# Kernel optimization log

Measured on AMD Instinct MI355X. Metric: run time of the kernel, lower is better.

The kernel has to match this reference:

```python
import jax, jax.numpy as jnp
import numpy as np

N_HEAD = 16
N_FEAT = 1024
D_K = N_FEAT // N_HEAD


def setup_inputs() -> dict:
    key = jax.random.key(0)
    ks = jax.random.split(key, 12)
    B, T, F = 4, 2048, N_FEAT
    s = 1.0 / np.sqrt(F)
    return {
        "query": jax.random.normal(ks[0], (B, T, F), dtype=jnp.float32),
        "key": jax.random.normal(ks[1], (B, T, F), dtype=jnp.float32),
        "value": jax.random.normal(ks[2], (B, T, F), dtype=jnp.float32),
        "mask": jnp.ones((B, 1, T), dtype=jnp.int32),
        "Wq": jax.random.normal(ks[3], (F, F), dtype=jnp.float32) * s,
        "bq": jax.random.normal(ks[4], (F,), dtype=jnp.float32) * 0.01,
        "Wk": jax.random.normal(ks[5], (F, F), dtype=jnp.float32) * s,
        "bk": jax.random.normal(ks[6], (F,), dtype=jnp.float32) * 0.01,
        "Wv": jax.random.normal(ks[7], (F, F), dtype=jnp.float32) * s,
        "bv": jax.random.normal(ks[8], (F,), dtype=jnp.float32) * 0.01,
        "Wo": jax.random.normal(ks[9], (F, F), dtype=jnp.float32) * s,
        "bo": jax.random.normal(ks[10], (F,), dtype=jnp.float32) * 0.01,
    }


def reference(query, key, value, mask, Wq, bq, Wk, bk, Wv, bv, Wo, bo):
    B, Tq, F = query.shape
    Tk = key.shape[1]
    h, dk = N_HEAD, D_K
    # torch nn.Linear: y = x @ W.T + b ; then view [B,T,h,dk] and transpose to [B,h,T,dk]
    q = (query @ Wq.T + bq).reshape(B, Tq, h, dk).transpose(0, 2, 1, 3)
    k = (key @ Wk.T + bk).reshape(B, Tk, h, dk).transpose(0, 2, 1, 3)
    v = (value @ Wv.T + bv).reshape(B, Tk, h, dk).transpose(0, 2, 1, 3)
    scale = 1.0 / np.sqrt(dk).astype(np.float32)
    scores = jnp.einsum("bhqd,bhkd->bhqk", q, k) * scale  # [B,h,Tq,Tk]
    # mask [B,1,Tk] -> unsqueeze(1) -> [B,1,1,Tk], True where mask == 0 (padded)
    pad = (mask[:, None, :, :] == 0)
    min_value = jnp.finfo(scores.dtype).min
    scores = jnp.where(pad, min_value, scores)
    atten = jax.nn.softmax(scores, axis=-1)
    atten = jnp.where(pad, 0.0, atten)
    # dropout_rate = 0.0 (eval): identity
    x = jnp.einsum("bhqk,bhkd->bhqd", atten, v)  # [B,h,Tq,dk]
    x = x.transpose(0, 2, 1, 3).reshape(B, Tq, h * dk)
    return x @ Wo.T + bo
```

## Files before the change

kernel.cpp:

```cpp
#include <hip/hip_runtime.h>
#include <hip/hip_bf16.h>


typedef unsigned short u16;
typedef unsigned long long u64;
typedef __attribute__((ext_vector_type(8))) short short8;
typedef __attribute__((ext_vector_type(4))) float f32x4;
typedef __attribute__((ext_vector_type(16))) float f32x16;
typedef __attribute__((ext_vector_type(4))) unsigned int u32x4;

#define GLOAD16(g, l) __builtin_amdgcn_global_load_lds( \
    (const __attribute__((address_space(1))) unsigned int*)(g), \
    (__attribute__((address_space(3))) unsigned int*)(l), 16, 0, 0)

__device__ __forceinline__ u16 f2bf(float x) {
  unsigned int u = __float_as_uint(x);
  return (u16)((u + 0x7fffu + ((u >> 16) & 1u)) >> 16);
}

__device__ __forceinline__ float fexp2(float x) {
#if __has_builtin(__builtin_amdgcn_exp2f)
  return __builtin_amdgcn_exp2f(x);
#else
  return exp2f(x);
#endif
}

__device__ __forceinline__ unsigned cvtpk(float lo, float hi) {
  unsigned r;
  asm("v_cvt_pk_bf16_f32 %0, %1, %2" : "=v"(r) : "v"(lo), "v"(hi));
  return r;
}

struct CvtArgs {
  const float* src[4];
  u16* dst[4];
};

__global__ __launch_bounds__(256) void cvt_multi(CvtArgs a, int shift) {
  const int id = blockIdx.x * 256 + threadIdx.x;
  const int seg = id >> shift;
  const int off = id & ((1 << shift) - 1);
  float4 v = ((const float4*)a.src[seg])[off];
  ushort4 o;
  o.x = f2bf(v.x); o.y = f2bf(v.y); o.z = f2bf(v.z); o.w = f2bf(v.w);
  ((ushort4*)a.dst[seg])[off] = o;
}

template <int EPI>
__global__ __launch_bounds__(256) void gemm_bt(const u16* __restrict__ A,
                                               const u16* __restrict__ Bw,
                                               const float* __restrict__ bias,
                                               void* __restrict__ Cout,
                                               float scale) {
  __shared__ u16 As[128 * 64];
  __shared__ u16 Bs[128 * 64];
  const int t = threadIdx.x;
  const int lane = t & 63;
  const int w = t >> 6;
  const int wm = w >> 1, wn = w & 1;
  const int l15 = lane & 15, l4 = lane >> 4;

  const int bid = blockIdx.x;
  const int swz = (bid & 7) * 64 + (bid >> 3);
  const int brow = swz >> 3;
  const int bcol = swz & 7;

  f32x4 acc[4][4] = {};

  const int srow = t >> 3;
  const int sbyte = (t & 7) * 16;

  for (int kt = 0; kt < 16; ++kt) {
    const int k0 = kt * 64;
    __syncthreads();
#pragma unroll
    for (int i = 0; i < 4; ++i) {
      const int r = i * 32 + srow;
      const int sb = sbyte ^ ((r & 7) << 4);
      GLOAD16((const char*)(A + (size_t)(brow * 128 + r) * 1024 + k0) + sb,
              &As[(i * 4096 + t * 16) >> 1]);
      GLOAD16((const char*)(Bw + (size_t)(bcol * 128 + r) * 1024 + k0) + sb,
              &Bs[(i * 4096 + t * 16) >> 1]);
    }
    __syncthreads();
#pragma unroll
    for (int kf = 0; kf < 2; ++kf) {
      short8 af[4], bfv[4];
#pragma unroll
      for (int mi = 0; mi < 4; ++mi) {
        const int r = wm * 64 + mi * 16 + l15;
        const int byt = r * 128 + ((kf * 64 + l4 * 16) ^ ((r & 7) << 4));
        af[mi] = *(const short8*)&As[byt >> 1];
      }
#pragma unroll
      for (int ni = 0; ni < 4; ++ni) {
        const int r = wn * 64 + ni * 16 + l15;
        const int byt = r * 128 + ((kf * 64 + l4 * 16) ^ ((r & 7) << 4));
        bfv[ni] = *(const short8*)&Bs[byt >> 1];
      }
#pragma unroll
      for (int mi = 0; mi < 4; ++mi)
#pragma unroll
        for (int ni = 0; ni < 4; ++ni)
          acc[mi][ni] = __builtin_amdgcn_mfma_f32_16x16x32_bf16(
              af[mi], bfv[ni], acc[mi][ni], 0, 0, 0);
    }
  }

#pragma unroll
  for (int ni = 0; ni < 4; ++ni) {
    const int n = bcol * 128 + wn * 64 + ni * 16 + l15;
    const float bn = bias[n];
#pragma unroll
    for (int mi = 0; mi < 4; ++mi) {
      const int mb = brow * 128 + wm * 64 + mi * 16 + l4 * 4;
#pragma unroll
      for (int r = 0; r < 4; ++r) {
        const float v = acc[mi][ni][r] + bn;
        const int m = mb + r;
        const int b_ = m >> 11, tok = m & 2047, h_ = n >> 6, d = n & 63;
        if (EPI == 0) {
          ((u16*)Cout)[(((size_t)(b_ * 16 + h_) * 2048 + tok) << 6) + d] = f2bf(v * scale);
        } else if (EPI == 2) {
          ((u16*)Cout)[(((size_t)(b_ * 16 + h_) * 64 + d) << 11) + tok] = f2bf(v);
        } else {
          ((float*)Cout)[(size_t)m * 1024 + n] = v;
        }
      }
    }
  }
}

__global__ __launch_bounds__(256, 4) void attn_fwd4(const u16* __restrict__ Q,
                                                    const u16* __restrict__ Kp,
                                                    const u16* __restrict__ Vt,
                                                    const int* __restrict__ mask,
                                                    u16* __restrict__ ctx) {
  __shared__ u16 Ks[2][64 * 64];
  __shared__ u16 Vs[2][64 * 64];

  const int t = threadIdx.x, lane = t & 63, w = t >> 6;
  const int q31 = lane & 31, hi = lane >> 5;

  const int bid = blockIdx.x;
  const int swz = (bid & 7) * 128 + (bid >> 3);
  const int bh = swz >> 4;
  const int b_ = bh >> 4, h_ = bh & 15;
  const int q0 = (swz & 15) * 128 + w * 32;
  const size_t headO = (size_t)bh * 131072;

  short8 qf[4];
  const u16* qrow = Q + headO + (size_t)(q0 + q31) * 64 + hi * 8;
#pragma unroll
  for (int ds = 0; ds < 4; ++ds) qf[ds] = *(const short8*)(qrow + ds * 16);

  const int srow = t >> 3;
  const int sbyte = (t & 7) * 16;

#define STAGE_KV(bufi, kb)                                                      \
  {                                                                             \
    _Pragma("unroll") for (int i = 0; i < 2; ++i) {                             \
      const int r = i * 32 + srow;                                              \
      const int sb = sbyte ^ ((r & 7) << 4);                                    \
      GLOAD16((const char*)(Kp + headO + (size_t)((kb) + r) * 64) + sb,         \
              &Ks[bufi][(i * 4096 + t * 16) >> 1]);                             \
      GLOAD16((const char*)(Vt + headO + (size_t)r * 2048 + (kb)) + sb,         \
              &Vs[bufi][(i * 4096 + t * 16) >> 1]);                             \
    }                                                                           \
  }

#define PACK(sv, pfa, pfb)                                                      \
  {                                                                             \
    const unsigned w0 = cvtpk(sv[0], sv[1]),   w1 = cvtpk(sv[2], sv[3]);        \
    const unsigned w2 = cvtpk(sv[4], sv[5]),   w3 = cvtpk(sv[6], sv[7]);        \
    const unsigned w4 = cvtpk(sv[8], sv[9]),   w5 = cvtpk(sv[10], sv[11]);      \
    const unsigned w6 = cvtpk(sv[12], sv[13]), w7 = cvtpk(sv[14], sv[15]);      \
    const unsigned x0 = (unsigned)__shfl_xor((int)(hi ? w0 : w2), 32);          \
    const unsigned x1 = (unsigned)__shfl_xor((int)(hi ? w1 : w3), 32);          \
    const unsigned y0 = (unsigned)__shfl_xor((int)(hi ? w4 : w6), 32);          \
    const unsigned y1 = (unsigned)__shfl_xor((int)(hi ? w5 : w7), 32);          \
    u32x4 fa = hi ? (u32x4){x0, x1, w2, w3} : (u32x4){w0, w1, x0, x1};          \
    u32x4 fb = hi ? (u32x4){y0, y1, w6, w7} : (u32x4){w4, w5, y0, y1};          \
    pfa = __builtin_bit_cast(short8, fa);                                       \
    pfb = __builtin_bit_cast(short8, fb);                                       \
  }

  f32x16 oacc0 = {}, oacc1 = {};
  float l_run = 0.f;
  const int kcol = hi * 16;
  const int rswz = (q31 & 7) << 4;

  STAGE_KV(0, 0);
  int mk = mask[b_ * 2048 + lane];
  __syncthreads();

  int buf = 0;
  for (int kt = 0; kt < 32; ++kt) {
    const int kb = kt * 64;
    if (kt + 1 < 32) STAGE_KV(buf ^ 1, kb + 64);
    const int mk_next = (kt + 1 < 32) ? mask[b_ * 2048 + kb + 64 + lane] : 0;
    const u64 bits = __ballot(mk != 0);

    f32x16 s0 = {}, s1 = {};
    __builtin_amdgcn_s_setprio(1);
#pragma unroll
    for (int ds = 0; ds < 4; ++ds) {
      const int cb = (ds * 32 + kcol) ^ rswz;
      short8 ka0 = *(const short8*)&Ks[buf][(q31 * 128 + cb) >> 1];
      short8 ka1 = *(const short8*)&Ks[buf][((32 + q31) * 128 + cb) >> 1];
      s0 = __builtin_amdgcn_mfma_f32_32x32x16_bf16(ka0, qf[ds], s0, 0, 0, 0);
      s1 = __builtin_amdgcn_mfma_f32_32x32x16_bf16(ka1, qf[ds], s1, 0, 0, 0);
    }
    __builtin_amdgcn_s_setprio(0);

    if (bits == ~0ull) {
#pragma unroll
      for (int r = 0; r < 16; ++r) { s0[r] = fexp2(s0[r]); s1[r] = fexp2(s1[r]); }
    } else {
#pragma unroll
      for (int r = 0; r < 16; ++r) {
        const int k0 = (r & 3) + 8 * (r >> 2) + 4 * hi;
        s0[r] = ((bits >> k0) & 1)        ? fexp2(s0[r]) : 0.f;
        s1[r] = ((bits >> (k0 + 32)) & 1) ? fexp2(s1[r]) : 0.f;
      }
    }

    float ra = 0.f, rb = 0.f;
#pragma unroll
    for (int r = 0; r < 16; r += 2) { ra += s0[r] + s1[r]; rb += s0[r + 1] + s1[r + 1]; }
    float rs = ra + rb;
    rs += __shfl_xor(rs, 32);
    l_run += rs;

    short8 pf[4];
    PACK(s0, pf[0], pf[1]);
    PACK(s1, pf[2], pf[3]);

    __builtin_amdgcn_s_setprio(1);
#pragma unroll
    for (int ks = 0; ks < 4; ++ks) {
      const int cb = (ks * 32 + kcol) ^ rswz;
      short8 va0 = *(const short8*)&Vs[buf][(q31 * 128 + cb) >> 1];
      short8 va1 = *(const short8*)&Vs[buf][((32 + q31) * 128 + cb) >> 1];
      oacc0 = __builtin_amdgcn_mfma_f32_32x32x16_bf16(va0, pf[ks], oacc0, 0, 0, 0);
      oacc1 = __builtin_amdgcn_mfma_f32_32x32x16_bf16(va1, pf[ks], oacc1, 0, 0, 0);
    }
    __builtin_amdgcn_s_setprio(0);

    mk = mk_next;
    __syncthreads();
    buf ^= 1;
  }
#undef STAGE_KV

  const float inv = l_run > 0.f ? 1.f / l_run : 0.f;
  const int tok = q0 + q31;
  u16* crow = ctx + ((size_t)b_ * 2048 + tok) * 1024 + h_ * 64 + 4 * hi;
#pragma unroll
  for (int g = 0; g < 4; ++g) {
    const unsigned a0 = cvtpk(oacc0[4 * g + 0] * inv, oacc0[4 * g + 1] * inv);
    const unsigned a1 = cvtpk(oacc0[4 * g + 2] * inv, oacc0[4 * g + 3] * inv);
    *(uint2*)(crow + 8 * g) = make_uint2(a0, a1);
    const unsigned b0 = cvtpk(oacc1[4 * g + 0] * inv, oacc1[4 * g + 1] * inv);
    const unsigned b1 = cvtpk(oacc1[4 * g + 2] * inv, oacc1[4 * g + 3] * inv);
    *(uint2*)(crow + 32 + 8 * g) = make_uint2(b0, b1);
  }
}

extern "C" void kernel_launch(void* const* d_in, const int* in_sizes, int n_in,
                              void* d_out, int out_size, void* d_ws, size_t ws_size,
                              hipStream_t stream) {
  const float* q_in = (const float*)d_in[0];
  const float* k_in = (const float*)d_in[1];
  const float* v_in = (const float*)d_in[2];
  const int*   mask = (const int*)d_in[3];
  const float* Wq = (const float*)d_in[4];
  const float* bq = (const float*)d_in[5];
  const float* Wk = (const float*)d_in[6];
  const float* bk = (const float*)d_in[7];
  const float* Wv = (const float*)d_in[8];
  const float* bv = (const float*)d_in[9];
  const float* Wo = (const float*)d_in[10];
  const float* bo = (const float*)d_in[11];
  float* out = (float*)d_out;

  char* ws = (char*)d_ws;
  u16* xq = (u16*)(ws);
  u16* xk = (u16*)(ws + 16777216);
  u16* xv = (u16*)(ws + 33554432);
  u16* Qp = (u16*)(ws + 50331648);
  u16* Kp = (u16*)(ws + 67108864);
  u16* Vtb = (u16*)(ws + 83886080);
  u16* wqb = (u16*)(ws + 100663296);
  u16* wkb = (u16*)(ws + 102760448);
  u16* wvb = (u16*)(ws + 104857600);
  u16* wob = (u16*)(ws + 106954752);
  u16* ctx = xk;

  CvtArgs big;
  big.src[0] = q_in; big.src[1] = k_in; big.src[2] = v_in; big.src[3] = v_in;
  big.dst[0] = xq;   big.dst[1] = xk;   big.dst[2] = xv;   big.dst[3] = xv;
  cvt_multi<<<3 * 8192, 256, 0, stream>>>(big, 21);
  CvtArgs wts;
  wts.src[0] = Wq;  wts.src[1] = Wk;  wts.src[2] = Wv;  wts.src[3] = Wo;
  wts.dst[0] = wqb; wts.dst[1] = wkb; wts.dst[2] = wvb; wts.dst[3] = wob;
  cvt_multi<<<4 * 1024, 256, 0, stream>>>(wts, 18);

  const float C_SCALE = 0.18033688011112042f;
  gemm_bt<0><<<512, 256, 0, stream>>>(xq, wqb, bq, Qp, C_SCALE);
  gemm_bt<0><<<512, 256, 0, stream>>>(xk, wkb, bk, Kp, 1.0f);
  gemm_bt<2><<<512, 256, 0, stream>>>(xv, wvb, bv, Vtb, 1.0f);

  attn_fwd4<<<1024, 256, 0, stream>>>(Qp, Kp, Vtb, mask, ctx);

  gemm_bt<1><<<512, 256, 0, stream>>>(ctx, wob, bo, out, 1.0f);
}
```

Baseline: 241.2 us.

## Process 64 query rows per wave in attention to reuse K/V fragments

The attention kernel now assigns 64 query rows per wave (256 per block) instead of 32, holding two Q fragment sets and four output accumulators. Each K and V fragment read from LDS feeds two MFMAs, halving LDS traffic and global K/V staging per query, and the block count halves to 512. In exchange, register pressure roughly doubles (launch bounds lowered to 2 blocks/CU) and fewer blocks reduce occupancy and latency hiding.

After: 227.5 us. 1.06x faster.

```diff
diff --git a/kernel.cpp b/kernel.cpp
--- a/kernel.cpp
+++ b/kernel.cpp
@@ -132,7 +132,7 @@
   }
 }
 
-__global__ __launch_bounds__(256, 4) void attn_fwd4(const u16* __restrict__ Q,
+__global__ __launch_bounds__(256, 2) void attn_fwd5(const u16* __restrict__ Q,
                                                     const u16* __restrict__ Kp,
                                                     const u16* __restrict__ Vt,
                                                     const int* __restrict__ mask,
@@ -144,16 +144,22 @@
   const int q31 = lane & 31, hi = lane >> 5;
 
   const int bid = blockIdx.x;
-  const int swz = (bid & 7) * 128 + (bid >> 3);
-  const int bh = swz >> 4;
+  const int swz = (bid & 7) * 64 + (bid >> 3);
+  const int bh = swz >> 3;
   const int b_ = bh >> 4, h_ = bh & 15;
-  const int q0 = (swz & 15) * 128 + w * 32;
+  const int q0 = (swz & 7) * 256 + w * 64;
   const size_t headO = (size_t)bh * 131072;
 
-  short8 qf[4];
-  const u16* qrow = Q + headO + (size_t)(q0 + q31) * 64 + hi * 8;
-#pragma unroll
-  for (int ds = 0; ds < 4; ++ds) qf[ds] = *(const short8*)(qrow + ds * 16);
+  short8 qfA[4], qfB[4];
+  {
+    const u16* qrowA = Q + headO + (size_t)(q0 + q31) * 64 + hi * 8;
+    const u16* qrowB = qrowA + 32 * 64;
+#pragma unroll
+    for (int ds = 0; ds < 4; ++ds) {
+      qfA[ds] = *(const short8*)(qrowA + ds * 16);
+      qfB[ds] = *(const short8*)(qrowB + ds * 16);
+    }
+  }
 
   const int srow = t >> 3;
   const int sbyte = (t & 7) * 16;
@@ -186,8 +192,8 @@
     pfb = __builtin_bit_cast(short8, fb);                                       \
   }
 
-  f32x16 oacc0 = {}, oacc1 = {};
-  float l_run = 0.f;
+  f32x16 oA0 = {}, oA1 = {}, oB0 = {}, oB1 = {};
+  float lA = 0.f, lB = 0.f;
   const int kcol = hi * 16;
   const int rswz = (q31 & 7) << 4;
 
@@ -202,51 +208,68 @@
     const int mk_next = (kt + 1 < 32) ? mask[b_ * 2048 + kb + 64 + lane] : 0;
     const u64 bits = __ballot(mk != 0);
 
-    f32x16 s0 = {}, s1 = {};
-    __builtin_amdgcn_s_setprio(1);
-#pragma unroll
-    for (int ds = 0; ds < 4; ++ds) {
-      const int cb = (ds * 32 + kcol) ^ rswz;
-      short8 ka0 = *(const short8*)&Ks[buf][(q31 * 128 + cb) >> 1];
-      short8 ka1 = *(const short8*)&Ks[buf][((32 + q31) * 128 + cb) >> 1];
-      s0 = __builtin_amdgcn_mfma_f32_32x32x16_bf16(ka0, qf[ds], s0, 0, 0, 0);
-      s1 = __builtin_amdgcn_mfma_f32_32x32x16_bf16(ka1, qf[ds], s1, 0, 0, 0);
-    }
-    __builtin_amdgcn_s_setprio(0);
-
-    if (bits == ~0ull) {
-#pragma unroll
-      for (int r = 0; r < 16; ++r) { s0[r] = fexp2(s0[r]); s1[r] = fexp2(s1[r]); }
-    } else {
-#pragma unroll
-      for (int r = 0; r < 16; ++r) {
-        const int k0 = (r & 3) + 8 * (r >> 2) + 4 * hi;
-        s0[r] = ((bits >> k0) & 1)        ? fexp2(s0[r]) : 0.f;
-        s1[r] = ((bits >> (k0 + 32)) & 1) ? fexp2(s1[r]) : 0.f;
-      }
-    }
-
-    float ra = 0.f, rb = 0.f;
-#pragma unroll
-    for (int r = 0; r < 16; r += 2) { ra += s0[r] + s1[r]; rb += s0[r + 1] + s1[r + 1]; }
-    float rs = ra + rb;
-    rs += __shfl_xor(rs, 32);
-    l_run += rs;
-
-    short8 pf[4];
-    PACK(s0, pf[0], pf[1]);
-    PACK(s1, pf[2], pf[3]);
-
-    __builtin_amdgcn_s_setprio(1);
-#pragma unroll
-    for (int ks = 0; ks < 4; ++ks) {
-      const int cb = (ks * 32 + kcol) ^ rswz;
-      short8 va0 = *(const short8*)&Vs[buf][(q31 * 128 + cb) >> 1];
-      short8 va1 = *(const short8*)&Vs[buf][((32 + q31) * 128 + cb) >> 1];
-      oacc0 = __builtin_amdgcn_mfma_f32_32x32x16_bf16(va0, pf[ks], oacc0, 0, 0, 0);
-      oacc1 = __builtin_amdgcn_mfma_f32_32x32x16_bf16(va1, pf[ks], oacc1, 0, 0, 0);
-    }
-    __builtin_amdgcn_s_setprio(0);
+#pragma unroll
+    for (int half = 0; half < 2; ++half) {
+      f32x16 sA = {}, sB = {};
+      __builtin_amdgcn_s_setprio(1);
+#pragma unroll
+      for (int ds = 0; ds < 4; ++ds) {
+        const int byt = (half * 32 + q31) * 128 + ((ds * 32 + kcol) ^ rswz);
+        short8 ka = *(const short8*)&Ks[buf][byt >> 1];
+        sA = __builtin_amdgcn_mfma_f32_32x32x16_bf16(ka, qfA[ds], sA, 0, 0, 0);
+        sB = __builtin_amdgcn_mfma_f32_32x32x16_bf16(ka, qfB[ds], sB, 0, 0, 0);
+      }
+      __builtin_amdgcn_s_setprio(0);
+
+      if (bits == ~0ull) {
+#pragma unroll
+        for (int r = 0; r < 16; ++r) { sA[r] = fexp2(sA[r]); sB[r] = fexp2(sB[r]); }
+      } else {
+#pragma unroll
+        for (int r = 0; r < 16; ++r) {
+          const int k0 = half * 32 + (r & 3) + 8 * (r >> 2) + 4 * hi;
+          const bool on = (bits >> k0) & 1;
+          sA[r] = on ? fexp2(sA[r]) : 0.f;
+          sB[r] = on ? fexp2(sB[r]) : 0.f;
+        }
+      }
+
+      {
+        float a0 = 0.f, a1 = 0.f, b0 = 0.f, b1 = 0.f;
+#pragma unroll
+        for (int r = 0; r < 16; r += 2) {
+          a0 += sA[r]; a1 += sA[r + 1];
+          b0 += sB[r]; b1 += sB[r + 1];
+        }
+        lA += a0 + a1;
+        lB += b0 + b1;
+      }
+
+      short8 pA0, pA1, pB0, pB1;
+      PACK(sA, pA0, pA1);
+      PACK(sB, pB0, pB1);
+
+      __builtin_amdgcn_s_setprio(1);
+      {
+        const int rb0 = q31 * 128, rb1 = (32 + q31) * 128;
+        const int c0 = (half * 64 + kcol) ^ rswz;
+        const int c1 = (half * 64 + 32 + kcol) ^ rswz;
+        short8 va;
+        va = *(const short8*)&Vs[buf][(rb0 + c0) >> 1];
+        oA0 = __builtin_amdgcn_mfma_f32_32x32x16_bf16(va, pA0, oA0, 0, 0, 0);
+        oB0 = __builtin_amdgcn_mfma_f32_32x32x16_bf16(va, pB0, oB0, 0, 0, 0);
+        va = *(const short8*)&Vs[buf][(rb0 + c1) >> 1];
+        oA0 = __builtin_amdgcn_mfma_f32_32x32x16_bf16(va, pA1, oA0, 0, 0, 0);
+        oB0 = __builtin_amdgcn_mfma_f32_32x32x16_bf16(va, pB1, oB0, 0, 0, 0);
+        va = *(const short8*)&Vs[buf][(rb1 + c0) >> 1];
+        oA1 = __builtin_amdgcn_mfma_f32_32x32x16_bf16(va, pA0, oA1, 0, 0, 0);
+        oB1 = __builtin_amdgcn_mfma_f32_32x32x16_bf16(va, pB0, oB1, 0, 0, 0);
+        va = *(const short8*)&Vs[buf][(rb1 + c1) >> 1];
+        oA1 = __builtin_amdgcn_mfma_f32_32x32x16_bf16(va, pA1, oA1, 0, 0, 0);
+        oB1 = __builtin_amdgcn_mfma_f32_32x32x16_bf16(va, pB1, oB1, 0, 0, 0);
+      }
+      __builtin_amdgcn_s_setprio(0);
+    }
 
     mk = mk_next;
     __syncthreads();
@@ -254,17 +277,28 @@
   }
 #undef STAGE_KV
 
-  const float inv = l_run > 0.f ? 1.f / l_run : 0.f;
-  const int tok = q0 + q31;
-  u16* crow = ctx + ((size_t)b_ * 2048 + tok) * 1024 + h_ * 64 + 4 * hi;
+  lA += __shfl_xor(lA, 32);
+  lB += __shfl_xor(lB, 32);
+  const float invA = lA > 0.f ? 1.f / lA : 0.f;
+  const float invB = lB > 0.f ? 1.f / lB : 0.f;
+  const int tokA = q0 + q31;
+  u16* crowA = ctx + ((size_t)b_ * 2048 + tokA) * 1024 + h_ * 64 + 4 * hi;
+  u16* crowB = crowA + 32 * 1024;
 #pragma unroll
   for (int g = 0; g < 4; ++g) {
-    const unsigned a0 = cvtpk(oacc0[4 * g + 0] * inv, oacc0[4 * g + 1] * inv);
-    const unsigned a1 = cvtpk(oacc0[4 * g + 2] * inv, oacc0[4 * g + 3] * inv);
-    *(uint2*)(crow + 8 * g) = make_uint2(a0, a1);
-    const unsigned b0 = cvtpk(oacc1[4 * g + 0] * inv, oacc1[4 * g + 1] * inv);
-    const unsigned b1 = cvtpk(oacc1[4 * g + 2] * inv, oacc1[4 * g + 3] * inv);
-    *(uint2*)(crow + 32 + 8 * g) = make_uint2(b0, b1);
+    unsigned u0, u1;
+    u0 = cvtpk(oA0[4 * g + 0] * invA, oA0[4 * g + 1] * invA);
+    u1 = cvtpk(oA0[4 * g + 2] * invA, oA0[4 * g + 3] * invA);
+    *(uint2*)(crowA + 8 * g) = make_uint2(u0, u1);
+    u0 = cvtpk(oA1[4 * g + 0] * invA, oA1[4 * g + 1] * invA);
+    u1 = cvtpk(oA1[4 * g + 2] * invA, oA1[4 * g + 3] * invA);
+    *(uint2*)(crowA + 32 + 8 * g) = make_uint2(u0, u1);
+    u0 = cvtpk(oB0[4 * g + 0] * invB, oB0[4 * g + 1] * invB);
+    u1 = cvtpk(oB0[4 * g + 2] * invB, oB0[4 * g + 3] * invB);
+    *(uint2*)(crowB + 8 * g) = make_uint2(u0, u1);
+    u0 = cvtpk(oB1[4 * g + 0] * invB, oB1[4 * g + 1] * invB);
+    u1 = cvtpk(oB1[4 * g + 2] * invB, oB1[4 * g + 3] * invB);
+    *(uint2*)(crowB + 32 + 8 * g) = make_uint2(u0, u1);
   }
 }
 
@@ -312,7 +346,7 @@
   gemm_bt<0><<<512, 256, 0, stream>>>(xk, wkb, bk, Kp, 1.0f);
   gemm_bt<2><<<512, 256, 0, stream>>>(xv, wvb, bv, Vtb, 1.0f);
 
-  attn_fwd4<<<1024, 256, 0, stream>>>(Qp, Kp, Vtb, mask, ctx);
+  attn_fwd5<<<512, 256, 0, stream>>>(Qp, Kp, Vtb, mask, ctx);
 
   gemm_bt<1><<<512, 256, 0, stream>>>(ctx, wob, bo, out, 1.0f);
 }
```
